# Performance work log

Measured on AMD Instinct MI355X. Metric: run time of the kernel, lower is better.

The kernel has to match this reference:

```python
import jax, jax.numpy as jnp
import numpy as np

KH = KW = 3
DIL = 1
PAD_H = DIL * (KH - 1) // 2
PAD_W = DIL * (KW - 1) // 2


def setup_inputs() -> dict:
    key = jax.random.key(0)
    k1, k2 = jax.random.split(key)
    b, c, h, w = 16, 64, 128, 128
    Dot = jax.random.normal(k1, (b, KH * KW, h, w), dtype=jnp.float32)
    V = jax.random.normal(k2, (b, c, h, w), dtype=jnp.float32)
    return {"Dot": Dot, "V": V}


def reference(Dot, V):
    # output[b,c,y,x] = sum_{i,j} Dot[b, i*KW+j, y, x] * V_padded[b, c, y+i*DIL, x+j*DIL]
    b, c, h, w = V.shape
    Vp = jnp.pad(V, ((0, 0), (0, 0), (PAD_H, PAD_H), (PAD_W, PAD_W)))
    out = jnp.zeros_like(V)
    for i in range(KH):
        for j in range(KW):
            k = i * KW + j  # unfold ordering: row-major over kernel window
            out = out + Dot[:, k:k + 1] * Vp[:, :, i * DIL:i * DIL + h, j * DIL:j * DIL + w]
    return out
```

## Files before the change

### kernel.cpp

```cpp
#include <hip/hip_runtime.h>


#define HH 128
#define WW 128
#define CC 64
#define KK 9

typedef float f4 __attribute__((ext_vector_type(4)));

__device__ __forceinline__ void accum3(f4& o, float vl, const f4& vm, float vr,
                                       const f4& d0, const f4& d1, const f4& d2)
{
    o.x += d0.x * vl   + d1.x * vm.x + d2.x * vm.y;
    o.y += d0.y * vm.x + d1.y * vm.y + d2.y * vm.z;
    o.z += d0.z * vm.y + d1.z * vm.z + d2.z * vm.w;
    o.w += d0.w * vm.z + d1.w * vm.w + d2.w * vr;
}

__global__ __launch_bounds__(256) void msa_conv2d_kernel(
    const float* __restrict__ Dot,
    const float* __restrict__ V,
    float* __restrict__ out)
{
    const int n  = blockIdx.x;
    const int L  = (n & 7) * 512 + (n >> 3);
    const int b  = L >> 8;
    const int r2 = L & 255;
    const int ys = r2 >> 3;
    const int cg = r2 & 7;
    const int y0 = ys * 4;

    const int tid = threadIdx.x;
    const int xq  = tid & 31;
    const int tc  = tid >> 5;
    const int c   = cg * 8 + tc;
    const int x0  = xq * 4;

    const float* vC = V   + (((size_t)b * CC + c) * HH) * WW + x0;
    const float* dC = Dot + ((size_t)b * KK) * (HH * WW) + x0;
    float*       oC = out + (((size_t)b * CC + c) * HH) * WW + x0;

    const f4 z4 = {0.f, 0.f, 0.f, 0.f};

    f4 r[6];
    r[0] = (y0 > 0)      ? *reinterpret_cast<const f4*>(vC + (size_t)(y0 - 1) * WW) : z4;
    #pragma unroll
    for (int i = 0; i < 4; ++i)
        r[i + 1] =         *reinterpret_cast<const f4*>(vC + (size_t)(y0 + i) * WW);
    r[5] = (y0 + 4 < HH) ? *reinterpret_cast<const f4*>(vC + (size_t)(y0 + 4) * WW) : z4;

    float lo[6], hi[6];
    #pragma unroll
    for (int i = 0; i < 6; ++i) {
        lo[i] = __shfl_up(r[i].w, 1, 32);
        hi[i] = __shfl_down(r[i].x, 1, 32);
    }
    if (xq == 0) {
        #pragma unroll
        for (int i = 0; i < 6; ++i) lo[i] = 0.f;
    }
    if (xq == 31) {
        #pragma unroll
        for (int i = 0; i < 6; ++i) hi[i] = 0.f;
    }

    #pragma unroll
    for (int y = 0; y < 4; ++y) {
        const float* dRow = dC + (size_t)(y0 + y) * WW;
        f4 w[KK];
        #pragma unroll
        for (int k = 0; k < KK; ++k)
            w[k] = *reinterpret_cast<const f4*>(dRow + (size_t)k * (HH * WW));

        f4 o = z4;
        accum3(o, lo[y    ], r[y    ], hi[y    ], w[0], w[1], w[2]);
        accum3(o, lo[y + 1], r[y + 1], hi[y + 1], w[3], w[4], w[5]);
        accum3(o, lo[y + 2], r[y + 2], hi[y + 2], w[6], w[7], w[8]);

        *reinterpret_cast<f4*>(oC + (size_t)(y0 + y) * WW) = o;
    }
}

extern "C" void kernel_launch(void* const* d_in, const int* in_sizes, int n_in,
                              void* d_out, int out_size, void* d_ws, size_t ws_size,
                              hipStream_t stream)
{
    const float* Dot = (const float*)d_in[0];
    const float* V   = (const float*)d_in[1];
    float* out       = (float*)d_out;

    msa_conv2d_kernel<<<dim3(4096), 256, 0, stream>>>(Dot, V, out);
}
```

Before: 33.73 us.

## Stage Dot tile in LDS via async loads and reuse across sixteen channels

```diff
diff --git a/kernel.cpp b/kernel.cpp
--- a/kernel.cpp
+++ b/kernel.cpp
@@ -5,6 +5,7 @@
 #define WW 128
 #define CC 64
 #define KK 9
+#define NT 4
 
 typedef float f4 __attribute__((ext_vector_type(4)));
 
@@ -22,62 +23,125 @@
     const float* __restrict__ V,
     float* __restrict__ out)
 {
-    const int n  = blockIdx.x;
-    const int L  = (n & 7) * 512 + (n >> 3);
-    const int b  = L >> 8;
-    const int r2 = L & 255;
-    const int ys = r2 >> 3;
-    const int cg = r2 & 7;
-    const int y0 = ys * 4;
+    __shared__ float dotS[8][KK][WW];
+
+    const int n   = blockIdx.x;
+    const int L   = (n & 7) * 128 + (n >> 3);
+    const int b   = L >> 6;
+    const int rem = L & 63;
+    const int yb  = rem >> 2;
+    const int chq = rem & 3;
+    const int yB  = yb * 8;
 
     const int tid = threadIdx.x;
-    const int xq  = tid & 31;
+    const int tx  = tid & 31;
     const int tc  = tid >> 5;
-    const int c   = cg * 8 + tc;
-    const int x0  = xq * 4;
+    const int x0  = tx * 4;
 
-    const float* vC = V   + (((size_t)b * CC + c) * HH) * WW + x0;
-    const float* dC = Dot + ((size_t)b * KK) * (HH * WW) + x0;
-    float*       oC = out + (((size_t)b * CC + c) * HH) * WW + x0;
+    const int c0 = chq * 16 + tc;
+    const int c1 = c0 + 8;
+
+    const float* vC0 = V + (((size_t)b * CC + c0) * HH) * WW + x0;
+    const float* vC1 = V + (((size_t)b * CC + c1) * HH) * WW + x0;
+    float*       oC0 = out + (((size_t)b * CC + c0) * HH) * WW + x0;
+    float*       oC1 = out + (((size_t)b * CC + c1) * HH) * WW + x0;
 
     const f4 z4 = {0.f, 0.f, 0.f, 0.f};
+    auto loadRow = [&](const float* base, int row) -> f4 {
+        return (row >= 0 && row < HH)
+             ? *reinterpret_cast<const f4*>(base + (size_t)row * WW) : z4;
+    };
 
-    f4 r[6];
-    r[0] = (y0 > 0)      ? *reinterpret_cast<const f4*>(vC + (size_t)(y0 - 1) * WW) : z4;
+    f4 w0[4], w1[4];
     #pragma unroll
-    for (int i = 0; i < 4; ++i)
-        r[i + 1] =         *reinterpret_cast<const f4*>(vC + (size_t)(y0 + i) * WW);
-    r[5] = (y0 + 4 < HH) ? *reinterpret_cast<const f4*>(vC + (size_t)(y0 + 4) * WW) : z4;
-
-    float lo[6], hi[6];
-    #pragma unroll
-    for (int i = 0; i < 6; ++i) {
-        lo[i] = __shfl_up(r[i].w, 1, 32);
-        hi[i] = __shfl_down(r[i].x, 1, 32);
-    }
-    if (xq == 0) {
-        #pragma unroll
-        for (int i = 0; i < 6; ++i) lo[i] = 0.f;
-    }
-    if (xq == 31) {
-        #pragma unroll
-        for (int i = 0; i < 6; ++i) hi[i] = 0.f;
+    for (int i = 0; i < 4; ++i) {
+        w0[i] = loadRow(vC0, yB - 1 + i);
+        w1[i] = loadRow(vC1, yB - 1 + i);
     }
 
+    {
+        float* ldsBase = &dotS[0][0][0];
+        #pragma unroll
+        for (int rnd = 0; rnd < 9; ++rnd) {
+            const int t  = tid + rnd * 256;
+            const int yy = t / 288;
+            const int rm = t - yy * 288;
+            const int k  = rm >> 5;
+            const int x4 = rm & 31;
+            const float* src = Dot + (((size_t)b * KK + k) * HH + (yB + yy)) * WW + x4 * 4;
+            __builtin_amdgcn_global_load_lds(
+                (const __attribute__((address_space(1))) void*)src,
+                (__attribute__((address_space(3))) void*)(ldsBase + (size_t)t * 4),
+                16, 0, 0);
+        }
+    }
+    __syncthreads();
+
     #pragma unroll
-    for (int y = 0; y < 4; ++y) {
-        const float* dRow = dC + (size_t)(y0 + y) * WW;
-        f4 w[KK];
+    for (int t = 0; t < NT; ++t) {
+        const int y0 = yB + t * 2;
+
+        f4 p00 = z4, p01 = z4, p10 = z4, p11 = z4;
+        if (t < NT - 1) {
+            p00 = loadRow(vC0, y0 + 3);
+            p01 = loadRow(vC0, y0 + 4);
+            p10 = loadRow(vC1, y0 + 3);
+            p11 = loadRow(vC1, y0 + 4);
+        }
+
+        float l0[4], h0[4], l1[4], h1[4];
         #pragma unroll
-        for (int k = 0; k < KK; ++k)
-            w[k] = *reinterpret_cast<const f4*>(dRow + (size_t)k * (HH * WW));
+        for (int i = 0; i < 4; ++i) {
+            l0[i] = __shfl_up(w0[i].w, 1, 32);  h0[i] = __shfl_down(w0[i].x, 1, 32);
+            l1[i] = __shfl_up(w1[i].w, 1, 32);  h1[i] = __shfl_down(w1[i].x, 1, 32);
+        }
+        if (tx == 0) {
+            #pragma unroll
+            for (int i = 0; i < 4; ++i) { l0[i] = 0.f; l1[i] = 0.f; }
+        }
+        if (tx == 31) {
+            #pragma unroll
+            for (int i = 0; i < 4; ++i) { h0[i] = 0.f; h1[i] = 0.f; }
+        }
 
-        f4 o = z4;
-        accum3(o, lo[y    ], r[y    ], hi[y    ], w[0], w[1], w[2]);
-        accum3(o, lo[y + 1], r[y + 1], hi[y + 1], w[3], w[4], w[5]);
-        accum3(o, lo[y + 2], r[y + 2], hi[y + 2], w[6], w[7], w[8]);
+        {
+            f4 dA[KK];
+            #pragma unroll
+            for (int k = 0; k < KK; ++k)
+                dA[k] = *reinterpret_cast<const f4*>(&dotS[t * 2][k][x0]);
 
-        *reinterpret_cast<f4*>(oC + (size_t)(y0 + y) * WW) = o;
+            f4 oA0 = z4, oA1 = z4;
+            accum3(oA0, l0[0], w0[0], h0[0], dA[0], dA[1], dA[2]);
+            accum3(oA0, l0[1], w0[1], h0[1], dA[3], dA[4], dA[5]);
+            accum3(oA0, l0[2], w0[2], h0[2], dA[6], dA[7], dA[8]);
+            accum3(oA1, l1[0], w1[0], h1[0], dA[0], dA[1], dA[2]);
+            accum3(oA1, l1[1], w1[1], h1[1], dA[3], dA[4], dA[5]);
+            accum3(oA1, l1[2], w1[2], h1[2], dA[6], dA[7], dA[8]);
+            *reinterpret_cast<f4*>(oC0 + (size_t)y0 * WW) = oA0;
+            *reinterpret_cast<f4*>(oC1 + (size_t)y0 * WW) = oA1;
+        }
+
+        {
+            f4 dB[KK];
+            #pragma unroll
+            for (int k = 0; k < KK; ++k)
+                dB[k] = *reinterpret_cast<const f4*>(&dotS[t * 2 + 1][k][x0]);
+
+            f4 oB0 = z4, oB1 = z4;
+            accum3(oB0, l0[1], w0[1], h0[1], dB[0], dB[1], dB[2]);
+            accum3(oB0, l0[2], w0[2], h0[2], dB[3], dB[4], dB[5]);
+            accum3(oB0, l0[3], w0[3], h0[3], dB[6], dB[7], dB[8]);
+            accum3(oB1, l1[1], w1[1], h1[1], dB[0], dB[1], dB[2]);
+            accum3(oB1, l1[2], w1[2], h1[2], dB[3], dB[4], dB[5]);
+            accum3(oB1, l1[3], w1[3], h1[3], dB[6], dB[7], dB[8]);
+            *reinterpret_cast<f4*>(oC0 + (size_t)(y0 + 1) * WW) = oB0;
+            *reinterpret_cast<f4*>(oC1 + (size_t)(y0 + 1) * WW) = oB1;
+        }
+
+        if (t < NT - 1) {
+            w0[0] = w0[2]; w0[1] = w0[3]; w0[2] = p00; w0[3] = p01;
+            w1[0] = w1[2]; w1[1] = w1[3]; w1[2] = p10; w1[3] = p11;
+        }
     }
 }
 
@@ -89,5 +153,5 @@
     const float* V   = (const float*)d_in[1];
     float* out       = (float*)d_out;
 
-    msa_conv2d_kernel<<<dim3(4096), 256, 0, stream>>>(Dot, V, out);
+    msa_conv2d_kernel<<<dim3(1024), 256, 0, stream>>>(Dot, V, out);
 }
```

Measured after the change: 27.99 us. 1.2x faster.
